# Performance work log

Measured on AMD Instinct MI355X. Metric: run time of the kernel, lower is better.

## Reference

```python
import jax, jax.numpy as jnp
import numpy as np

LAYERS, HIDDEN, FFN, HEADS = 4, 512, 1024, 4
B, S = 2, 2048
HD = HIDDEN // HEADS  # head size = 128
SCALE_BASE = 512.0
EPS = 1e-5


def _xpos(x, downscale):
    # x: (B, H, S, hd). Faithful to torchscale XPOS with offset=0.
    seq, hd = x.shape[-2], x.shape[-1]
    half = hd // 2
    s = (jnp.arange(0, hd, 2, dtype=jnp.float32) + 0.4 * hd) / (1.4 * hd)  # (half,)
    pos = jnp.arange(seq, dtype=jnp.float32)
    scale = s[None, :] ** (pos[:, None] / SCALE_BASE)  # (S, half)
    inv_freq = 1.0 / (10000.0 ** (jnp.arange(half, dtype=jnp.float32) / half))
    ang = pos[:, None] * inv_freq[None, :]  # (S, half)
    sin, cos = jnp.sin(ang), jnp.cos(ang)
    if downscale:
        scale = 1.0 / scale
    sin_s = jnp.repeat(sin * scale, 2, axis=-1)  # duplicate_interleave -> (S, hd)
    cos_s = jnp.repeat(cos * scale, 2, axis=-1)
    x1, x2 = x[..., ::2], x[..., 1::2]
    rot = jnp.stack([-x2, x1], axis=-1).reshape(x.shape)  # rotate_every_two
    return x * cos_s + rot * sin_s


def _decay_mask(seq, heads):
    gammas = 1.0 - jnp.exp(jnp.linspace(jnp.log(1.0 / 32.0), jnp.log(1.0 / 512.0), heads))
    n = jnp.arange(seq)[:, None]
    m = jnp.arange(seq)[None, :]
    diff = n - m
    pw = gammas[:, None, None] ** jnp.maximum(diff, 0)[None].astype(jnp.float32)
    return jnp.where(diff[None] >= 0, pw, 0.0)  # (H, S, S)


def _ln(x, w, b):
    mu = x.mean(-1, keepdims=True)
    var = x.var(-1, keepdims=True)
    return (x - mu) / jnp.sqrt(var + EPS) * w + b


def _gn(y, w, b, heads):
    # GroupNorm(heads, D) applied on rows of (B*S, D)
    bb, ss, d = y.shape
    hs = d // heads
    yr = y.reshape(bb, ss, heads, hs)
    mu = yr.mean(-1, keepdims=True)
    var = yr.var(-1, keepdims=True)
    yn = ((yr - mu) / jnp.sqrt(var + EPS)).reshape(bb, ss, d)
    return yn * w + b


def setup_inputs() -> dict:
    key = jax.random.key(0)
    ks = jax.random.split(key, 17)
    sc = 1.0 / HIDDEN
    inp = {
        'X': jax.random.normal(ks[0], (B, S, HIDDEN), dtype=jnp.float32),
        'Wq': jax.random.normal(ks[1], (LAYERS, HEADS, HIDDEN, HD), dtype=jnp.float32) * sc,
        'Wk': jax.random.normal(ks[2], (LAYERS, HEADS, HIDDEN, HD), dtype=jnp.float32) * sc,
        'Wv': jax.random.normal(ks[3], (LAYERS, HEADS, HIDDEN, HD), dtype=jnp.float32) * sc,
        'Wg': jax.random.normal(ks[4], (LAYERS, HIDDEN, HIDDEN), dtype=jnp.float32) * sc,
        'Wo': jax.random.normal(ks[5], (LAYERS, HIDDEN, HIDDEN), dtype=jnp.float32) * sc,
        'gn_w': jnp.ones((LAYERS, HIDDEN), dtype=jnp.float32),
        'gn_b': jnp.zeros((LAYERS, HIDDEN), dtype=jnp.float32),
        'ln1_w': jnp.ones((LAYERS, HIDDEN), dtype=jnp.float32),
        'ln1_b': jnp.zeros((LAYERS, HIDDEN), dtype=jnp.float32),
        'ln2_w': jnp.ones((LAYERS, HIDDEN), dtype=jnp.float32),
        'ln2_b': jnp.zeros((LAYERS, HIDDEN), dtype=jnp.float32),
        'f1_w': jax.random.normal(ks[6], (LAYERS, HIDDEN, FFN), dtype=jnp.float32) * (1.0 / np.sqrt(HIDDEN)),
        'f1_b': jnp.zeros((LAYERS, FFN), dtype=jnp.float32),
        'f2_w': jax.random.normal(ks[7], (LAYERS, FFN, HIDDEN), dtype=jnp.float32) * (1.0 / np.sqrt(FFN)),
        'f2_b': jnp.zeros((LAYERS, HIDDEN), dtype=jnp.float32),
    }
    return inp


def reference(X, Wq, Wk, Wv, Wg, Wo, gn_w, gn_b, ln1_w, ln1_b, ln2_w, ln2_b, f1_w, f1_b, f2_w, f2_b):
    bb, ss, d = X.shape
    Dm = _decay_mask(ss, HEADS)  # (H, S, S)
    for i in range(LAYERS):
        Xn = _ln(X, ln1_w[i], ln1_b[i])
        Q = jnp.einsum('bsd,hde->bhse', Xn, Wq[i])
        K = jnp.einsum('bsd,hde->bhse', Xn, Wk[i])
        V = jnp.einsum('bsd,hde->bhse', Xn, Wv[i])
        Q = _xpos(Q, downscale=False)
        K = _xpos(K, downscale=True)
        att = jnp.einsum('bhse,bhte->bhst', Q, K) * Dm[None]
        ret = jnp.einsum('bhst,bhte->bhse', att, V)  # (B,H,S,hd)
        Yh = ret.transpose(0, 2, 1, 3).reshape(bb, ss, d)
        Yg = _gn(Yh, gn_w[i], gn_b[i], HEADS)
        msr = (jax.nn.silu(Xn @ Wg[i]) * Yg) @ Wo[i]
        Y = msr + X
        Yn = _ln(Y, ln2_w[i], ln2_b[i])
        X = jax.nn.gelu(Yn @ f1_w[i] + f1_b[i], approximate=False) @ f2_w[i] + f2_b[i] + Y
    return X
```

## Files before the change

### kernel.cpp

```cpp
#include <hip/hip_runtime.h>
#include <hip/hip_bf16.h>
#include <cstdint>
#include <cstddef>

#define SEQ_ 2048

typedef __bf16 v8bf __attribute__((ext_vector_type(8)));
typedef float v4f __attribute__((ext_vector_type(4)));

__device__ __forceinline__ unsigned short f2bf(float f) {
  unsigned u = __float_as_uint(f);
  return (unsigned short)((u + 0x7FFFu + ((u >> 16) & 1u)) >> 16);
}
__device__ __forceinline__ float bf2f(unsigned short h) {
  return __uint_as_float(((unsigned)h) << 16);
}
__device__ __forceinline__ float silu_(float x) { return x / (1.f + expf(-x)); }
__device__ __forceinline__ float gelu_(float x) { return 0.5f * x * (1.f + erff(x * 0.70710678118654752f)); }

__device__ __forceinline__ void gl_lds16(const void* g, void* l) {
  __builtin_amdgcn_global_load_lds((const __attribute__((address_space(1))) void*)g,
                                   (__attribute__((address_space(3))) void*)l, 16, 0, 0);
}

template <int ROWS>
__device__ __forceinline__ void stage_t(const unsigned short* gsrc, int ldk, char* lds, int tid) {
  const int wid = tid >> 6;
#pragma unroll
  for (int p = 0; p < ROWS / 32; ++p) {
    const int L = p * 256 + tid;
    const int row = L >> 3, slot = L & 7;
    gl_lds16((const char*)(gsrc + (size_t)row * ldk) + ((slot * 16) ^ ((row & 7) << 4)),
             lds + (p * 256 + wid * 64) * 16);
  }
}

template <int NROWS>
__device__ __forceinline__ void stage_rows(const char* gbase, int srow, char* lds, int tid) {
  const int wid = tid >> 6;
#pragma unroll
  for (int q = 0; q < NROWS / 16; ++q) {
    const int L = q * 256 + tid;
    const int row = L >> 4;
    const int slot = L & 15;
    gl_lds16(gbase + (size_t)row * srow + ((slot * 16) ^ ((row & 7) << 4)),
             lds + (q * 256 + wid * 64) * 16);
  }
}

__global__ __launch_bounds__(256) void setup_k(const float* __restrict__ Wq, const float* __restrict__ Wk,
                                               const float* __restrict__ Wv, const float* __restrict__ Wg,
                                               const float* __restrict__ Wo, const float* __restrict__ f1w,
                                               const float* __restrict__ f2w, float* __restrict__ tab,
                                               unsigned short* __restrict__ WTQ, unsigned short* __restrict__ WTO,
                                               unsigned short* __restrict__ WF1, unsigned short* __restrict__ WF2) {
  const int b = blockIdx.x, tid = threadIdx.x;
  if (b < 512) {
    const int idx = b * 256 + tid;
    const int pos = idx >> 6, i = idx & 63;
    const float si = (2.f * (float)i + 51.2f) * (1.f / 179.2f);
    const float sc = powf(si, (float)pos * (1.f / 512.f));
    const float invf = powf(10000.f, -(float)i * (1.f / 64.f));
    const float ang = (float)pos * invf;
    const float cs = cosf(ang), sn = sinf(ang);
    tab[idx] = cs * sc;
    tab[131072 + idx] = sn * sc;
    tab[262144 + idx] = cs / sc;
    tab[393216 + idx] = sn / sc;
    return;
  }
  __shared__ float t[64][65];
  const float* src;
  unsigned short* dst;
  int ldn, ldk;
  int b2 = b - 512;
  if (b2 < 768) {
    const int l = b2 / 192, r = b2 % 192, sec = r / 64, r2 = r % 64, h = r2 >> 4, tt = r2 & 15;
    const int kt = tt >> 1, et = tt & 1;
    const float* W = (sec == 0) ? Wq : (sec == 1) ? Wk : Wv;
    src = W + (((size_t)(l * 4 + h) * 512 + kt * 64) * 128 + et * 64);
    ldn = 128;
    dst = WTQ + (size_t)l * 1048576 + (size_t)(sec * 512 + h * 128 + et * 64) * 512 + kt * 64;
    ldk = 512;
  } else if (b2 < 1024) {
    b2 -= 768;
    const int l = b2 >> 6, tt = b2 & 63, kt = tt >> 3, nt = tt & 7;
    src = Wg + (size_t)l * 262144 + (size_t)kt * 64 * 512 + nt * 64;
    ldn = 512;
    dst = WTQ + (size_t)l * 1048576 + (size_t)(1536 + nt * 64) * 512 + kt * 64;
    ldk = 512;
  } else if (b2 < 1280) {
    b2 -= 1024;
    const int l = b2 >> 6, tt = b2 & 63, kt = tt >> 3, nt = tt & 7;
    src = Wo + (size_t)l * 262144 + (size_t)kt * 64 * 512 + nt * 64;
    ldn = 512;
    dst = WTO + (size_t)l * 262144 + (size_t)nt * 64 * 512 + kt * 64;
    ldk = 512;
  } else if (b2 < 1792) {
    b2 -= 1280;
    const int l = b2 >> 7, tt = b2 & 127, kt = tt >> 4, nt = tt & 15;
    src = f1w + (size_t)l * 524288 + (size_t)kt * 64 * 1024 + nt * 64;
    ldn = 1024;
    dst = WF1 + (size_t)l * 524288 + (size_t)nt * 64 * 512 + kt * 64;
    ldk = 512;
  } else {
    b2 -= 1792;
    const int l = b2 >> 7, tt = b2 & 127, kt = tt >> 3, nt = tt & 7;
    src = f2w + (size_t)l * 524288 + (size_t)kt * 64 * 512 + nt * 64;
    ldn = 512;
    dst = WF2 + (size_t)l * 524288 + (size_t)nt * 64 * 1024 + kt * 64;
    ldk = 1024;
  }
#pragma unroll
  for (int p = 0; p < 4; ++p) {
    const int idx = p * 256 + tid;
    const int kr = idx >> 4, c4 = (idx & 15) * 4;
    const float4 v = *(const float4*)(src + (size_t)kr * ldn + c4);
    t[kr][c4] = v.x; t[kr][c4 + 1] = v.y; t[kr][c4 + 2] = v.z; t[kr][c4 + 3] = v.w;
  }
  __syncthreads();
#pragma unroll
  for (int p = 0; p < 2; ++p) {
    const int idx = p * 256 + tid;
    const int nr = idx >> 3, k8 = (idx & 7) * 8;
    unsigned short o[8];
#pragma unroll
    for (int j = 0; j < 8; ++j) o[j] = f2bf(t[k8 + j][nr]);
    uint4 pk;
    pk.x = o[0] | ((unsigned)o[1] << 16);
    pk.y = o[2] | ((unsigned)o[3] << 16);
    pk.z = o[4] | ((unsigned)o[5] << 16);
    pk.w = o[6] | ((unsigned)o[7] << 16);
    *(uint4*)(dst + (size_t)nr * ldk + k8) = pk;
  }
}

__global__ __launch_bounds__(256) void ln_bf_k(const float* __restrict__ x, const float* __restrict__ w,
                                               const float* __restrict__ bv, unsigned short* __restrict__ out) {
  const int row = blockIdx.x * 4 + (threadIdx.x >> 6);
  const int lane = threadIdx.x & 63;
  const float* xr = x + (size_t)row * 512 + lane * 8;
  const float4 v0 = *(const float4*)xr;
  const float4 v1 = *(const float4*)(xr + 4);
  float va[8] = {v0.x, v0.y, v0.z, v0.w, v1.x, v1.y, v1.z, v1.w};
  float s = 0.f, ss = 0.f;
#pragma unroll
  for (int j = 0; j < 8; ++j) { s += va[j]; ss += va[j] * va[j]; }
#pragma unroll
  for (int o = 1; o < 64; o <<= 1) { s += __shfl_xor(s, o); ss += __shfl_xor(ss, o); }
  const float mu = s * (1.f / 512.f);
  const float var = ss * (1.f / 512.f) - mu * mu;
  const float rstd = rsqrtf(var + 1e-5f);
  const int c = lane * 8;
  unsigned short o16[8];
#pragma unroll
  for (int j = 0; j < 8; ++j) o16[j] = f2bf((va[j] - mu) * rstd * w[c + j] + bv[c + j]);
  uint4 pk;
  pk.x = o16[0] | ((unsigned)o16[1] << 16);
  pk.y = o16[2] | ((unsigned)o16[3] << 16);
  pk.z = o16[4] | ((unsigned)o16[5] << 16);
  pk.w = o16[6] | ((unsigned)o16[7] << 16);
  *(uint4*)(out + (size_t)row * 512 + c) = pk;
}

template <int BM, int BN, int EPI>
__global__ __launch_bounds__(256) void mm_k(
    const unsigned short* __restrict__ A, const unsigned short* __restrict__ Bt, const int K,
    const float* __restrict__ t_qc, const float* __restrict__ t_qs,
    const float* __restrict__ t_kc, const float* __restrict__ t_ks,
    unsigned short* __restrict__ o_q, unsigned short* __restrict__ o_k,
    unsigned short* __restrict__ o_ktw, unsigned short* __restrict__ o_vt,
    unsigned short* __restrict__ o_g0,
    const float* __restrict__ auxf, const float* __restrict__ auxf2,
    float* __restrict__ o_f32, unsigned short* __restrict__ o_bf16) {
  constexpr int MR = BM / 32, NR = BN / 32;
  constexpr int BMB = BM * 128, BNB = BN * 128;
  __shared__ __align__(16) char smem[2 * (BMB + BNB)];
  const int tid = threadIdx.x, lane = tid & 63, wid = tid >> 6;
  const int wr = wid >> 1, wc = wid & 1;
  const int l15 = lane & 15, l4 = lane >> 4;
  const int m0 = blockIdx.x * BM, n0 = blockIdx.y * BN;
  const int N = gridDim.y * BN;
  v4f acc[MR][NR];
#pragma unroll
  for (int i = 0; i < MR; ++i)
#pragma unroll
    for (int j = 0; j < NR; ++j) acc[i][j] = v4f{0.f, 0.f, 0.f, 0.f};

  const unsigned short* Ab = A + (size_t)m0 * K;
  const unsigned short* Bb = Bt + (size_t)n0 * K;
  const int NT = K >> 6;
  int cur = 0;
  stage_t<BM>(Ab, K, smem, tid);
  stage_t<BN>(Bb, K, smem + 2 * BMB, tid);
  __syncthreads();
  for (int t = 0; t < NT; ++t) {
    if (t + 1 < NT) {
      stage_t<BM>(Ab + (t + 1) * 64, K, smem + (cur ^ 1) * BMB, tid);
      stage_t<BN>(Bb + (t + 1) * 64, K, smem + 2 * BMB + (cur ^ 1) * BNB, tid);
    }
    const char* Ac = smem + cur * BMB;
    const char* Bc = smem + 2 * BMB + cur * BNB;
#pragma unroll
    for (int ks = 0; ks < 2; ++ks) {
      v8bf af[MR], bfv[NR];
#pragma unroll
      for (int i = 0; i < MR; ++i) {
        const int row = wr * (BM / 2) + i * 16 + l15;
        af[i] = *(const v8bf*)(Ac + row * 128 + ((ks * 64 + l4 * 16) ^ ((row & 7) << 4)));
      }
#pragma unroll
      for (int j = 0; j < NR; ++j) {
        const int row = wc * (BN / 2) + j * 16 + l15;
        bfv[j] = *(const v8bf*)(Bc + row * 128 + ((ks * 64 + l4 * 16) ^ ((row & 7) << 4)));
      }
#pragma unroll
      for (int i = 0; i < MR; ++i)
#pragma unroll
        for (int j = 0; j < NR; ++j)
          acc[i][j] = __builtin_amdgcn_mfma_f32_16x16x32_bf16(af[i], bfv[j], acc[i][j], 0, 0, 0);
    }
    __syncthreads();
    cur ^= 1;
  }

  if constexpr (EPI == 0) {
    const int sec = n0 >> 9;
    const int h = (n0 >> 7) & 3;
    const int srow0 = m0 & (SEQ_ - 1);
    const int bh = ((m0 >> 11) << 2) | h;
    unsigned short* sT = (unsigned short*)smem;
    const float gamma = 1.f - expf(-3.4657359028f - 0.9241962407f * (float)h);
    const float l2g = log2f(gamma);
#pragma unroll
    for (int i = 0; i < MR; ++i) {
#pragma unroll
      for (int r = 0; r < 4; ++r) {
        const int rl = wr * (BM / 2) + i * 16 + l4 * 4 + r;
        const int srow = srow0 + rl;
        const float wk = (sec == 1) ? exp2f(l2g * (float)(127 - (rl & 127))) : 0.f;
#pragma unroll
        for (int j = 0; j < NR; ++j) {
          const int cl = wc * (BN / 2) + j * 16 + l15;
          float v = acc[i][j][r];
          if (sec <= 1) {
            const float p = __shfl_xor(v, 1);
            const float* ct = (sec == 0) ? t_qc : t_kc;
            const float* st = (sec == 0) ? t_qs : t_ks;
            const float c_ = ct[srow * 64 + (cl >> 1)];
            const float s_ = st[srow * 64 + (cl >> 1)];
            const float o = (lane & 1) ? fmaf(v, c_, p * s_) : fmaf(v, c_, -p * s_);
            if (sec == 0) {
              o_q[((size_t)bh * SEQ_ + srow) * 128 + cl] = f2bf(o);
            } else {
              o_k[((size_t)bh * SEQ_ + srow) * 128 + cl] = f2bf(o);
              sT[cl * 136 + rl] = f2bf(o * wk);
            }
          } else if (sec == 2) {
            sT[cl * 136 + rl] = f2bf(v);
          } else {
            o_g0[(size_t)(m0 + rl) * 512 + cl] = f2bf(v);
          }
        }
      }
    }
    if (sec == 1 || sec == 2) {
      __syncthreads();
      unsigned short* dstT = ((sec == 1) ? o_ktw : o_vt) + (size_t)bh * 128 * SEQ_ + srow0;
#pragma unroll
      for (int u = 0; u < 8; ++u) {
        const int idx = u * 256 + tid;
        const int d = idx >> 4, j8 = idx & 15;
        *(v8bf*)(dstT + (size_t)d * SEQ_ + j8 * 8) = *(const v8bf*)(sT + d * 136 + j8 * 8);
      }
    }
  } else {
#pragma unroll
    for (int i = 0; i < MR; ++i) {
#pragma unroll
      for (int r = 0; r < 4; ++r) {
        const int row = m0 + wr * (BM / 2) + i * 16 + l4 * 4 + r;
#pragma unroll
        for (int j = 0; j < NR; ++j) {
          const int col = n0 + wc * (BN / 2) + j * 16 + l15;
          const float v = acc[i][j][r];
          if constexpr (EPI == 1) {
            o_f32[(size_t)row * 512 + col] = v + auxf[(size_t)row * 512 + col];
          } else if constexpr (EPI == 2) {
            o_bf16[(size_t)row * N + col] = f2bf(gelu_(v + auxf[col]));
          } else {
            o_f32[(size_t)row * 512 + col] = v + auxf[col] + auxf2[(size_t)row * 512 + col];
          }
        }
      }
    }
  }
}

__global__ __launch_bounds__(256) void ret1_k(const unsigned short* __restrict__ VT,
                                              const unsigned short* __restrict__ KTw,
                                              float* __restrict__ U) {
  __shared__ __align__(16) char lA[32768];
  __shared__ __align__(16) char lB[32768];
  const int bh = blockIdx.x, c = blockIdx.y;
  const int tid = threadIdx.x, lane = tid & 63, wid = tid >> 6;
  const int wr = wid >> 1, wc = wid & 1;
  const int l15 = lane & 15, l4 = lane >> 4;
  stage_rows<128>((const char*)(VT + (size_t)bh * 128 * SEQ_ + (size_t)c * 128), SEQ_ * 2, lA, tid);
  stage_rows<128>((const char*)(KTw + (size_t)bh * 128 * SEQ_ + (size_t)c * 128), SEQ_ * 2, lB, tid);
  __syncthreads();
  v4f acc[4][4];
#pragma unroll
  for (int i = 0; i < 4; ++i)
#pragma unroll
    for (int j = 0; j < 4; ++j) acc[i][j] = v4f{0.f, 0.f, 0.f, 0.f};
#pragma unroll
  for (int ks = 0; ks < 4; ++ks) {
    v8bf af[4], bfv[4];
#pragma unroll
    for (int i = 0; i < 4; ++i) {
      const int ra = wr * 64 + i * 16 + l15;
      af[i] = *(const v8bf*)(lA + ra * 256 + ((ks * 64 + l4 * 16) ^ ((ra & 7) << 4)));
      const int rb = wc * 64 + i * 16 + l15;
      bfv[i] = *(const v8bf*)(lB + rb * 256 + ((ks * 64 + l4 * 16) ^ ((rb & 7) << 4)));
    }
#pragma unroll
    for (int i = 0; i < 4; ++i)
#pragma unroll
      for (int j = 0; j < 4; ++j)
        acc[i][j] = __builtin_amdgcn_mfma_f32_16x16x32_bf16(af[i], bfv[j], acc[i][j], 0, 0, 0);
  }
  float* ub = U + ((size_t)bh * 16 + c) * 16384;
#pragma unroll
  for (int i = 0; i < 4; ++i)
#pragma unroll
    for (int r = 0; r < 4; ++r) {
      const int rd = wr * 64 + i * 16 + l4 * 4 + r;
#pragma unroll
      for (int j = 0; j < 4; ++j) {
        const int ce = wc * 64 + j * 16 + l15;
        ub[rd * 128 + ce] = acc[i][j][r];
      }
    }
}

__global__ __launch_bounds__(256) void ret2_k(const float* __restrict__ U, unsigned short* __restrict__ Sb) {
  const int bh = blockIdx.x;
  const int idx = blockIdx.y * 256 + threadIdx.x;
  const int h = bh & 3;
  const float gamma = 1.f - expf(-3.4657359028f - 0.9241962407f * (float)h);
  const float g128 = exp2f(log2f(gamma) * 128.f);
  float s = 0.f;
#pragma unroll
  for (int c = 0; c < 16; ++c) {
    Sb[((size_t)bh * 16 + c) * 16384 + idx] = f2bf(s);
    s = s * g128 + U[((size_t)bh * 16 + c) * 16384 + idx];
  }
}

template <int HF>
__device__ __forceinline__ void ret3_body(
    const unsigned short* Qb, const unsigned short* Kb, const unsigned short* VTb,
    const unsigned short* Sb, const unsigned short* G0b, const float* gnw,
    const float* gnb, unsigned short* Gb, char* lA, char* lB, const float* dpw,
    float* rs, int bh, int c, int tid) {
  const int h = bh & 3, b = bh >> 2;
  const int lane = tid & 63, wid = tid >> 6;
  const int wr = wid >> 1, wc = wid & 1;
  const int l15 = lane & 15, l4 = lane >> 4;
  constexpr int NS = 2 + 2 * HF;
  constexpr int KS = 2 + 2 * HF;
  const int j0 = c * 128 + HF * 64;

  stage_rows<64>((const char*)(Qb + ((size_t)bh * SEQ_ + j0) * 128), 256, lA, tid);
  stage_rows<128>((const char*)(Sb + ((size_t)bh * 16 + c) * 16384), 256, lB, tid);
  __syncthreads();

  v4f acc[2][4];
#pragma unroll
  for (int i = 0; i < 2; ++i)
#pragma unroll
    for (int j = 0; j < 4; ++j) acc[i][j] = v4f{0.f, 0.f, 0.f, 0.f};
#pragma unroll
  for (int ks = 0; ks < 4; ++ks) {
    v8bf af[2], bfv[4];
#pragma unroll
    for (int i = 0; i < 2; ++i) {
      const int ra = wr * 32 + i * 16 + l15;
      af[i] = *(const v8bf*)(lA + ra * 256 + ((ks * 64 + l4 * 16) ^ ((ra & 7) << 4)));
    }
#pragma unroll
    for (int j = 0; j < 4; ++j) {
      const int rb = wc * 64 + j * 16 + l15;
      bfv[j] = *(const v8bf*)(lB + rb * 256 + ((ks * 64 + l4 * 16) ^ ((rb & 7) << 4)));
    }
#pragma unroll
    for (int i = 0; i < 2; ++i)
#pragma unroll
      for (int j = 0; j < 4; ++j)
        acc[i][j] = __builtin_amdgcn_mfma_f32_16x16x32_bf16(af[i], bfv[j], acc[i][j], 0, 0, 0);
  }
#pragma unroll
  for (int i = 0; i < 2; ++i)
#pragma unroll
    for (int r = 0; r < 4; ++r) {
      const float sc = dpw[HF * 64 + wr * 32 + i * 16 + l4 * 4 + r + 1];
#pragma unroll
      for (int j = 0; j < 4; ++j) acc[i][j][r] *= sc;
    }
  __syncthreads();
  if constexpr (HF == 0)
    stage_rows<64>((const char*)(Kb + ((size_t)bh * SEQ_ + c * 128) * 128), 256, lB, tid);
  else
    stage_rows<128>((const char*)(Kb + ((size_t)bh * SEQ_ + c * 128) * 128), 256, lB, tid);
  __syncthreads();

  v4f sacc[2][NS];
#pragma unroll
  for (int i = 0; i < 2; ++i)
#pragma unroll
    for (int j = 0; j < NS; ++j) sacc[i][j] = v4f{0.f, 0.f, 0.f, 0.f};
#pragma unroll
  for (int ks = 0; ks < 4; ++ks) {
    v8bf af[2], bfv[NS];
#pragma unroll
    for (int i = 0; i < 2; ++i) {
      const int ra = wr * 32 + i * 16 + l15;
      af[i] = *(const v8bf*)(lA + ra * 256 + ((ks * 64 + l4 * 16) ^ ((ra & 7) << 4)));
    }
#pragma unroll
    for (int j = 0; j < NS; ++j) {
      const int rb = wc * (16 * NS) + j * 16 + l15;
      bfv[j] = *(const v8bf*)(lB + rb * 256 + ((ks * 64 + l4 * 16) ^ ((rb & 7) << 4)));
    }
#pragma unroll
    for (int i = 0; i < 2; ++i)
#pragma unroll
      for (int j = 0; j < NS; ++j)
        sacc[i][j] = __builtin_amdgcn_mfma_f32_16x16x32_bf16(af[i], bfv[j], sacc[i][j], 0, 0, 0);
  }
  __syncthreads();

#pragma unroll
  for (int i = 0; i < 2; ++i)
#pragma unroll
    for (int r = 0; r < 4; ++r) {
      const int jl = wr * 32 + i * 16 + l4 * 4 + r;
#pragma unroll
      for (int j = 0; j < NS; ++j) {
        const int icol = wc * (16 * NS) + j * 16 + l15;
        const int d = HF * 64 + jl - icol;
        const float p = (d < 0) ? 0.f : sacc[i][j][r] * dpw[d];
        *(unsigned short*)(lA + jl * 256 + ((icol * 2) ^ ((jl & 7) << 4))) = f2bf(p);
      }
    }
  if constexpr (HF == 0)
    stage_t<128>(VTb + (size_t)bh * 128 * SEQ_ + (size_t)c * 128, SEQ_, lB, tid);
  else
    stage_rows<128>((const char*)(VTb + (size_t)bh * 128 * SEQ_ + (size_t)c * 128), SEQ_ * 2, lB, tid);
  __syncthreads();

#pragma unroll
  for (int ks = 0; ks < KS; ++ks) {
    v8bf af[2], bfv[4];
#pragma unroll
    for (int i = 0; i < 2; ++i) {
      const int ra = wr * 32 + i * 16 + l15;
      af[i] = *(const v8bf*)(lA + ra * 256 + ((ks * 64 + l4 * 16) ^ ((ra & 7) << 4)));
    }
#pragma unroll
    for (int j = 0; j < 4; ++j) {
      const int rb = wc * 64 + j * 16 + l15;
      if constexpr (HF == 0)
        bfv[j] = *(const v8bf*)(lB + rb * 128 + ((ks * 64 + l4 * 16) ^ ((rb & 7) << 4)));
      else
        bfv[j] = *(const v8bf*)(lB + rb * 256 + ((ks * 64 + l4 * 16) ^ ((rb & 7) << 4)));
    }
#pragma unroll
    for (int i = 0; i < 2; ++i)
#pragma unroll
      for (int j = 0; j < 4; ++j)
        acc[i][j] = __builtin_amdgcn_mfma_f32_16x16x32_bf16(af[i], bfv[j], acc[i][j], 0, 0, 0);
  }

#pragma unroll
  for (int i = 0; i < 2; ++i)
#pragma unroll
    for (int r = 0; r < 4; ++r) {
      const int jl = wr * 32 + i * 16 + l4 * 4 + r;
      float s1 = 0.f, s2 = 0.f;
#pragma unroll
      for (int j = 0; j < 4; ++j) { const float v = acc[i][j][r]; s1 += v; s2 += v * v; }
#pragma unroll
      for (int o = 1; o < 16; o <<= 1) { s1 += __shfl_xor(s1, o); s2 += __shfl_xor(s2, o); }
      if (l15 == 0) { rs[(wc * 64 + jl) * 2] = s1; rs[(wc * 64 + jl) * 2 + 1] = s2; }
    }
  __syncthreads();
#pragma unroll
  for (int i = 0; i < 2; ++i)
#pragma unroll
    for (int r = 0; r < 4; ++r) {
      const int jl = wr * 32 + i * 16 + l4 * 4 + r;
      const float s1 = rs[jl * 2] + rs[(64 + jl) * 2];
      const float s2 = rs[jl * 2 + 1] + rs[(64 + jl) * 2 + 1];
      const float mu = s1 * (1.f / 128.f);
      const float var = s2 * (1.f / 128.f) - mu * mu;
      const float rstd = rsqrtf(var + 1e-5f);
      const size_t t = (size_t)(b * SEQ_ + j0 + jl);
#pragma unroll
      for (int j = 0; j < 4; ++j) {
        const int dd = wc * 64 + j * 16 + l15;
        const int cc = h * 128 + dd;
        const float g0 = bf2f(G0b[t * 512 + cc]);
        float o = (acc[i][j][r] - mu) * rstd * gnw[cc] + gnb[cc];
        o *= silu_(g0);
        Gb[t * 512 + cc] = f2bf(o);
      }
    }
}

__global__ __launch_bounds__(256) void ret3_k(
    const unsigned short* __restrict__ Qb, const unsigned short* __restrict__ Kb,
    const unsigned short* __restrict__ VTb, const unsigned short* __restrict__ Sb,
    const unsigned short* __restrict__ G0b, const float* __restrict__ gnw,
    const float* __restrict__ gnb, unsigned short* __restrict__ Gb) {
  __shared__ __align__(16) char lA[16384];
  __shared__ __align__(16) char lB[32768];
  __shared__ float dpw[132];
  __shared__ float rs[128 * 2];
  const int bh = blockIdx.x;
  const int hf = blockIdx.y & 1, c = blockIdx.y >> 1;
  const int tid = threadIdx.x;
  const int h = bh & 3;
  const float gamma = 1.f - expf(-3.4657359028f - 0.9241962407f * (float)h);
  const float l2g = log2f(gamma);
  if (tid < 132) dpw[tid] = exp2f(l2g * (float)tid);
  if (hf == 0)
    ret3_body<0>(Qb, Kb, VTb, Sb, G0b, gnw, gnb, Gb, lA, lB, dpw, rs, bh, c, tid);
  else
    ret3_body<1>(Qb, Kb, VTb, Sb, G0b, gnw, gnb, Gb, lA, lB, dpw, rs, bh, c, tid);
}

extern "C" void kernel_launch(void* const* d_in, const int* in_sizes, int n_in,
                              void* d_out, int out_size, void* d_ws, size_t ws_size,
                              hipStream_t stream) {
  const float* X = (const float*)d_in[0];
  const float* Wq = (const float*)d_in[1];
  const float* Wk = (const float*)d_in[2];
  const float* Wv = (const float*)d_in[3];
  const float* Wg = (const float*)d_in[4];
  const float* Wo = (const float*)d_in[5];
  const float* gnw = (const float*)d_in[6];
  const float* gnb = (const float*)d_in[7];
  const float* ln1w = (const float*)d_in[8];
  const float* ln1b = (const float*)d_in[9];
  const float* ln2w = (const float*)d_in[10];
  const float* ln2b = (const float*)d_in[11];
  const float* f1w = (const float*)d_in[12];
  const float* f1b = (const float*)d_in[13];
  const float* f2w = (const float*)d_in[14];
  const float* f2b = (const float*)d_in[15];

  char* ws = (char*)d_ws;
  float* TAB = (float*)(ws + 0);
  unsigned short* WTQ = (unsigned short*)(ws + 2097152);
  unsigned short* WTO = (unsigned short*)(ws + 10485760);
  unsigned short* WF1 = (unsigned short*)(ws + 12582912);
  unsigned short* WF2 = (unsigned short*)(ws + 16777216);
  unsigned short* XNb = (unsigned short*)(ws + 20971520);
  unsigned short* Qb  = (unsigned short*)(ws + 25165824);
  unsigned short* Kb  = (unsigned short*)(ws + 29360128);
  unsigned short* KTw = (unsigned short*)(ws + 33554432);
  unsigned short* VTb = (unsigned short*)(ws + 37748736);
  unsigned short* G0b = (unsigned short*)(ws + 46137344);
  unsigned short* Sbf = (unsigned short*)(ws + 50331648);
  unsigned short* Gb  = (unsigned short*)(ws + 54525952);
  float* Y   = (float*)(ws + 58720256);
  float* XB  = (float*)(ws + 67108864);
  unsigned short* F1b = (unsigned short*)(ws + 75497472);
  float* U = (float*)(ws + 75497472);
  float* qc = TAB, * qs = TAB + 131072, * kc = TAB + 262144, * ks = TAB + 393216;

  setup_k<<<2816, 256, 0, stream>>>(Wq, Wk, Wv, Wg, Wo, f1w, f2w, TAB, WTQ, WTO, WF1, WF2);

  const float* Xcur = X;
  for (int l = 0; l < 4; ++l) {
    ln_bf_k<<<1024, 256, 0, stream>>>(Xcur, ln1w + l * 512, ln1b + l * 512, XNb);
    mm_k<128, 128, 0><<<dim3(32, 16), 256, 0, stream>>>(
        XNb, WTQ + (size_t)l * 2048 * 512, 512, qc, qs, kc, ks,
        Qb, Kb, KTw, VTb, G0b, nullptr, nullptr, nullptr, nullptr);
    ret1_k<<<dim3(8, 16), 256, 0, stream>>>(VTb, KTw, U);
    ret2_k<<<dim3(8, 64), 256, 0, stream>>>(U, Sbf);
    ret3_k<<<dim3(8, 32), 256, 0, stream>>>(Qb, Kb, VTb, Sbf, G0b,
                                            gnw + l * 512, gnb + l * 512, Gb);
    mm_k<128, 64, 1><<<dim3(32, 8), 256, 0, stream>>>(
        Gb, WTO + (size_t)l * 512 * 512, 512, nullptr, nullptr, nullptr, nullptr,
        nullptr, nullptr, nullptr, nullptr, nullptr, Xcur, nullptr, Y, nullptr);
    ln_bf_k<<<1024, 256, 0, stream>>>(Y, ln2w + l * 512, ln2b + l * 512, XNb);
    mm_k<128, 128, 2><<<dim3(32, 8), 256, 0, stream>>>(
        XNb, WF1 + (size_t)l * 1024 * 512, 512, nullptr, nullptr, nullptr, nullptr,
        nullptr, nullptr, nullptr, nullptr, nullptr, f1b + l * 1024, nullptr, nullptr, F1b);
    float* outX = (l == 3) ? (float*)d_out : XB;
    mm_k<128, 64, 3><<<dim3(32, 8), 256, 0, stream>>>(
        F1b, WF2 + (size_t)l * 512 * 1024, 1024, nullptr, nullptr, nullptr, nullptr,
        nullptr, nullptr, nullptr, nullptr, nullptr, f2b + l * 512, Y, outX, nullptr);
    Xcur = XB;
  }
}
```

Before: 505.2 us.

## Fuse chunk state computation and decay scan into one retention kernel

Merges the per-chunk K^T V product kernel and the decayed prefix-scan kernel into a single kernel. Each block owns 32 rows of the state and loops over the 16 chunks, keeping the running state in registers and writing the bf16 prefix directly. This removes the fp32 intermediate buffer round trip through global memory and one launch. In exchange the grid shrinks to 32 blocks that process chunks serially, which lowers parallelism.

```diff
diff --git a/kernel.cpp b/kernel.cpp
--- a/kernel.cpp
+++ b/kernel.cpp
@@ -297,64 +297,56 @@
   }
 }
 
-__global__ __launch_bounds__(256) void ret1_k(const unsigned short* __restrict__ VT,
-                                              const unsigned short* __restrict__ KTw,
-                                              float* __restrict__ U) {
-  __shared__ __align__(16) char lA[32768];
-  __shared__ __align__(16) char lB[32768];
-  const int bh = blockIdx.x, c = blockIdx.y;
+__global__ __launch_bounds__(256) void ret12_k(const unsigned short* __restrict__ VT,
+                                               const unsigned short* __restrict__ KTw,
+                                               unsigned short* __restrict__ Sb) {
+  __shared__ __align__(16) char lV[8192];
+  __shared__ __align__(16) char lK[32768];
+  const int bh = blockIdx.x, es = blockIdx.y * 32;
   const int tid = threadIdx.x, lane = tid & 63, wid = tid >> 6;
   const int wr = wid >> 1, wc = wid & 1;
   const int l15 = lane & 15, l4 = lane >> 4;
-  stage_rows<128>((const char*)(VT + (size_t)bh * 128 * SEQ_ + (size_t)c * 128), SEQ_ * 2, lA, tid);
-  stage_rows<128>((const char*)(KTw + (size_t)bh * 128 * SEQ_ + (size_t)c * 128), SEQ_ * 2, lB, tid);
-  __syncthreads();
-  v4f acc[4][4];
-#pragma unroll
-  for (int i = 0; i < 4; ++i)
-#pragma unroll
-    for (int j = 0; j < 4; ++j) acc[i][j] = v4f{0.f, 0.f, 0.f, 0.f};
-#pragma unroll
-  for (int ks = 0; ks < 4; ++ks) {
-    v8bf af[4], bfv[4];
-#pragma unroll
-    for (int i = 0; i < 4; ++i) {
-      const int ra = wr * 64 + i * 16 + l15;
-      af[i] = *(const v8bf*)(lA + ra * 256 + ((ks * 64 + l4 * 16) ^ ((ra & 7) << 4)));
-      const int rb = wc * 64 + i * 16 + l15;
-      bfv[i] = *(const v8bf*)(lB + rb * 256 + ((ks * 64 + l4 * 16) ^ ((rb & 7) << 4)));
-    }
-#pragma unroll
-    for (int i = 0; i < 4; ++i)
-#pragma unroll
-      for (int j = 0; j < 4; ++j)
-        acc[i][j] = __builtin_amdgcn_mfma_f32_16x16x32_bf16(af[i], bfv[j], acc[i][j], 0, 0, 0);
-  }
-  float* ub = U + ((size_t)bh * 16 + c) * 16384;
-#pragma unroll
-  for (int i = 0; i < 4; ++i)
-#pragma unroll
-    for (int r = 0; r < 4; ++r) {
-      const int rd = wr * 64 + i * 16 + l4 * 4 + r;
-#pragma unroll
-      for (int j = 0; j < 4; ++j) {
-        const int ce = wc * 64 + j * 16 + l15;
-        ub[rd * 128 + ce] = acc[i][j][r];
-      }
-    }
-}
-
-__global__ __launch_bounds__(256) void ret2_k(const float* __restrict__ U, unsigned short* __restrict__ Sb) {
-  const int bh = blockIdx.x;
-  const int idx = blockIdx.y * 256 + threadIdx.x;
   const int h = bh & 3;
   const float gamma = 1.f - expf(-3.4657359028f - 0.9241962407f * (float)h);
   const float g128 = exp2f(log2f(gamma) * 128.f);
-  float s = 0.f;
-#pragma unroll
+  const char* Vbase = (const char*)(VT + ((size_t)bh * 128 + es) * SEQ_);
+  const char* Kbase = (const char*)(KTw + (size_t)bh * 128 * SEQ_);
+  v4f st[4];
+#pragma unroll
+  for (int j = 0; j < 4; ++j) st[j] = v4f{0.f, 0.f, 0.f, 0.f};
   for (int c = 0; c < 16; ++c) {
-    Sb[((size_t)bh * 16 + c) * 16384 + idx] = f2bf(s);
-    s = s * g128 + U[((size_t)bh * 16 + c) * 16384 + idx];
+    stage_rows<32>(Vbase + (size_t)c * 256, SEQ_ * 2, lV, tid);
+    stage_rows<128>(Kbase + (size_t)c * 256, SEQ_ * 2, lK, tid);
+    __syncthreads();
+    v4f u[4];
+#pragma unroll
+    for (int j = 0; j < 4; ++j) u[j] = v4f{0.f, 0.f, 0.f, 0.f};
+#pragma unroll
+    for (int ks = 0; ks < 4; ++ks) {
+      const int ra = wr * 16 + l15;
+      const v8bf af = *(const v8bf*)(lV + ra * 256 + ((ks * 64 + l4 * 16) ^ ((ra & 7) << 4)));
+      v8bf bfv[4];
+#pragma unroll
+      for (int j = 0; j < 4; ++j) {
+        const int rb = wc * 64 + j * 16 + l15;
+        bfv[j] = *(const v8bf*)(lK + rb * 256 + ((ks * 64 + l4 * 16) ^ ((rb & 7) << 4)));
+      }
+#pragma unroll
+      for (int j = 0; j < 4; ++j)
+        u[j] = __builtin_amdgcn_mfma_f32_16x16x32_bf16(af, bfv[j], u[j], 0, 0, 0);
+    }
+    unsigned short* sc = Sb + ((size_t)bh * 16 + c) * 16384;
+#pragma unroll
+    for (int r = 0; r < 4; ++r) {
+      const int e = es + wr * 16 + l4 * 4 + r;
+#pragma unroll
+      for (int j = 0; j < 4; ++j) {
+        const int d = wc * 64 + j * 16 + l15;
+        sc[e * 128 + d] = f2bf(st[j][r]);
+        st[j][r] = st[j][r] * g128 + u[j][r];
+      }
+    }
+    __syncthreads();
   }
 }
 
@@ -578,7 +570,6 @@
   float* Y   = (float*)(ws + 58720256);
   float* XB  = (float*)(ws + 67108864);
   unsigned short* F1b = (unsigned short*)(ws + 75497472);
-  float* U = (float*)(ws + 75497472);
   float* qc = TAB, * qs = TAB + 131072, * kc = TAB + 262144, * ks = TAB + 393216;
 
   setup_k<<<2816, 256, 0, stream>>>(Wq, Wk, Wv, Wg, Wo, f1w, f2w, TAB, WTQ, WTO, WF1, WF2);
@@ -589,8 +580,7 @@
     mm_k<128, 128, 0><<<dim3(32, 16), 256, 0, stream>>>(
         XNb, WTQ + (size_t)l * 2048 * 512, 512, qc, qs, kc, ks,
         Qb, Kb, KTw, VTb, G0b, nullptr, nullptr, nullptr, nullptr);
-    ret1_k<<<dim3(8, 16), 256, 0, stream>>>(VTb, KTw, U);
-    ret2_k<<<dim3(8, 64), 256, 0, stream>>>(U, Sbf);
+    ret12_k<<<dim3(8, 4), 256, 0, stream>>>(VTb, KTw, Sbf);
     ret3_k<<<dim3(8, 32), 256, 0, stream>>>(Qb, Kb, VTb, Sbf, G0b,
                                             gnw + l * 512, gnb + l * 512, Gb);
     mm_k<128, 64, 1><<<dim3(32, 8), 256, 0, stream>>>(
```

Result: slower. 553.3 us (+9.5%).
